# Kernel optimization log

Hardware: AMD Instinct MI355X
Metric: run time of the kernel (lower is better)

The kernel has to match this reference:

```python
import jax, jax.numpy as jnp
import numpy as np

TEMPERATURE = 0.1
NORM_EPS = 1e-12  # torch F.normalize clamps the norm at 1e-12


def _l2_normalize(x):
    n = jnp.sqrt(jnp.sum(x * x, axis=-1, keepdims=True))
    return x / jnp.maximum(n, NORM_EPS)


def setup_inputs() -> dict:
    key = jax.random.key(0)
    k1, k2 = jax.random.split(key)
    feat = jax.random.normal(k1, (32, 384, 28, 28), dtype=jnp.float32)
    codebook = jax.random.normal(k2, (2048, 384), dtype=jnp.float32)
    return {"feat": feat, "codebook": codebook}


def reference(feat, codebook):
    # feat: (b, c, h, w); codebook: (K, c)
    b, c, h, w = feat.shape
    K = codebook.shape[0]

    f = jnp.transpose(feat, (0, 2, 3, 1))          # (b, h, w, c), unnormalized
    flat = f.reshape(-1, c)                        # (N, c)
    flat_n = _l2_normalize(flat)                   # normalize=True
    code = _l2_normalize(codebook)                 # (K, c)

    distance = (jnp.sum(flat_n * flat_n, axis=1, keepdims=True)
                + jnp.sum(code * code, axis=1)
                - 2.0 * (flat_n @ code.T))

    # hard assignment (is_weight_sum=False): gather nearest code
    idx = jnp.argmin(distance, axis=1)             # (N,)
    q = code[idx]                                  # (N, c) == one_hot(idx) @ code
    q = q.reshape(b, h, w, c)

    # straight-through: gradient flows to f, not the quantized values
    q_feat = f + jax.lax.stop_gradient(q - f)      # (b, h, w, c)
    q_feat = jnp.transpose(q_feat, (0, 3, 1, 2))   # (b, c, h, w)

    prob = jax.nn.softmax(-distance / TEMPERATURE, axis=1)  # (N, K)
    assignment = jnp.transpose(prob.reshape(b, h, w, K), (0, 3, 1, 2))  # (b, K, h, w)

    return (f, q_feat, assignment, distance)
```

## Files before the change

kernel.cpp:

```cpp
#include <hip/hip_runtime.h>

#define B_  32
#define C_  384
#define HW_ 784
#define N_  25088
#define K_  2048
#define PPX 112

#define OFF_F    0
#define OFF_Q    9633792
#define OFF_ASG  19267584
#define OFF_DIST 70647808

#define MARGIN 0.02f

typedef unsigned short u16;
typedef unsigned int u32;
typedef __attribute__((ext_vector_type(8))) short short8;
typedef __attribute__((ext_vector_type(4))) float floatx4;

static __device__ __forceinline__ u16 f2bf(float x) {
    u32 u = __builtin_bit_cast(u32, x);
    u32 r = (u + 0x7FFFu + ((u >> 16) & 1u)) >> 16;
    return (u16)r;
}

static __device__ __forceinline__ void gload_lds16(const void* g, void* l) {
    __builtin_amdgcn_global_load_lds(
        (const __attribute__((address_space(1))) unsigned int*)g,
        (__attribute__((address_space(3))) unsigned int*)l,
        16, 0, 0);
}

static __device__ __forceinline__ size_t qslot(int b, int s, int hw) {
    return ((size_t)b * C_ + s) * HW_ + hw;
}

__global__ __launch_bounds__(256) void k_code(const float* __restrict__ cb,
                                              float* __restrict__ code_n,
                                              u16* __restrict__ b_hi) {
    int row  = blockIdx.x * 4 + (threadIdx.x >> 6);
    int lane = threadIdx.x & 63;
    const float* src = cb + (size_t)row * C_;
    float v[6];
    float ss = 0.f;
#pragma unroll
    for (int i = 0; i < 6; ++i) { v[i] = src[lane + 64 * i]; ss += v[i] * v[i]; }
#pragma unroll
    for (int off = 32; off; off >>= 1) ss += __shfl_xor(ss, off, 64);
    float inv = 1.f / fmaxf(sqrtf(ss), 1e-12f);
#pragma unroll
    for (int i = 0; i < 6; ++i) {
        float vn = v[i] * inv;
        code_n[(size_t)row * C_ + lane + 64 * i] = vn;
        b_hi  [(size_t)row * C_ + lane + 64 * i] = f2bf(vn);
    }
}

__global__ __launch_bounds__(256) void k_prep(const float* __restrict__ feat,
                                              float* __restrict__ f_out,
                                              float* __restrict__ inv_n,
                                              u16* __restrict__ a_hi) {
    __shared__ float tile[C_][17];
    __shared__ float red[16][17];
    __shared__ float s_inv[16];
    int b   = blockIdx.y;
    int hw0 = blockIdx.x * 16;
    int tid = threadIdx.x;
    int px  = tid & 15, cq = tid >> 4;

#pragma unroll
    for (int it = 0; it < 24; ++it) {
        int c = cq + 16 * it;
        tile[c][px] = feat[((size_t)(b * C_ + c)) * HW_ + hw0 + px];
    }
    __syncthreads();
    float ss = 0.f;
#pragma unroll
    for (int q = 0; q < 24; ++q) {
        float v = tile[cq + 16 * q][px];
        ss = fmaf(v, v, ss);
    }
    red[cq][px] = ss;
    __syncthreads();
    if (tid < 16) {
        float tot = 0.f;
#pragma unroll
        for (int p = 0; p < 16; ++p) tot += red[p][tid];
        float inv = 1.f / fmaxf(sqrtf(tot), 1e-12f);
        s_inv[tid] = inv;
        inv_n[(size_t)b * HW_ + hw0 + tid] = inv;
    }
    __syncthreads();

    {
        int p2 = tid >> 4, cc = tid & 15;
        float* fb = f_out + ((size_t)(b * HW_ + hw0 + p2)) * C_;
#pragma unroll
        for (int it = 0; it < 6; ++it) {
            int c0 = cc * 4 + 64 * it;
            float4 v;
            v.x = tile[c0 + 0][p2];
            v.y = tile[c0 + 1][p2];
            v.z = tile[c0 + 2][p2];
            v.w = tile[c0 + 3][p2];
            *(float4*)(fb + c0) = v;
        }
    }
    {
        int p2 = tid >> 4, cc = tid & 15;
        float inv = s_inv[p2];
        u16* aptr = a_hi + ((size_t)(b * HW_ + hw0 + p2)) * C_;
#pragma unroll
        for (int it = 0; it < 12; ++it) {
            int c0 = 2 * cc + 32 * it;
            u16 h0 = f2bf(tile[c0][p2] * inv);
            u16 h1 = f2bf(tile[c0 + 1][p2] * inv);
            *(u32*)(aptr + c0) = (u32)h0 | ((u32)h1 << 16);
        }
    }
}

__global__ __launch_bounds__(256) void k_gemm(const u16* __restrict__ A,
                                              const u16* __restrict__ Bm,
                                              float* __restrict__ D) {
    __shared__ u16 As[2][128 * 32];
    __shared__ u16 Bs[2][128 * 32];
    int tid = threadIdx.x;
    int n0 = blockIdx.x * 128, m0 = blockIdx.y * 128;
    int w = tid >> 6, l = tid & 63;
    int wm = (w >> 1) * 64, wn = (w & 1) * 64;
    int q4 = l >> 4, r15 = l & 15;

    floatx4 acc[4][4];
#pragma unroll
    for (int i = 0; i < 4; ++i)
#pragma unroll
        for (int j = 0; j < 4; ++j) acc[i][j] = (floatx4)0.f;

    int srow = tid >> 2;
    int sp   = tid & 3;
    int fs   = (srow ^ (srow >> 2)) & 3;
    int kk0  = 8 * (sp ^ fs);

#define STAGE(buf, kt)                                                          \
    {                                                                           \
        _Pragma("unroll")                                                       \
        for (int q = 0; q < 2; ++q) {                                           \
            int row = q * 64 + srow;                                            \
            int off = (q * 256 + tid) * 16;                                     \
            gload_lds16(A  + (size_t)(m0 + row) * C_ + (kt) + kk0,              \
                        (char*)As[buf] + off);                                  \
            gload_lds16(Bm + (size_t)(n0 + row) * C_ + (kt) + kk0,              \
                        (char*)Bs[buf] + off);                                  \
        }                                                                       \
    }

    STAGE(0, 0);
    __syncthreads();

    const int slot = (q4 ^ ((r15 ^ (r15 >> 2)) & 3)) << 4;
#pragma unroll 1
    for (int t = 0; t < 12; ++t) {
        int cur = t & 1;
        if (t < 11) STAGE(cur ^ 1, (t + 1) * 32);
        const char* Ab = (const char*)As[cur];
        const char* Bb = (const char*)Bs[cur];
        short8 a[4], b[4];
#pragma unroll
        for (int i = 0; i < 4; ++i) {
            a[i] = *(const short8*)(Ab + (wm + i * 16 + r15) * 64 + slot);
            b[i] = *(const short8*)(Bb + (wn + i * 16 + r15) * 64 + slot);
        }
#pragma unroll
        for (int i = 0; i < 4; ++i)
#pragma unroll
            for (int j = 0; j < 4; ++j)
                acc[i][j] = __builtin_amdgcn_mfma_f32_16x16x32_bf16(a[i], b[j], acc[i][j], 0, 0, 0);
        __syncthreads();
    }

#pragma unroll
    for (int i = 0; i < 4; ++i) {
        int gm = m0 + wm + i * 16 + q4 * 4;
#pragma unroll
        for (int j = 0; j < 4; ++j) {
            int gn = n0 + wn + j * 16 + r15;
            float* p = D + (size_t)gm * K_ + gn;
#pragma unroll
            for (int r = 0; r < 4; ++r)
                p[(size_t)r * K_] = 2.f - 2.f * acc[i][j][r];
        }
    }
#undef STAGE
}

__global__ __launch_bounds__(256) void k_stats(const float* __restrict__ D,
                                               float2* __restrict__ srow) {
    int row = blockIdx.x * 4 + (threadIdx.x >> 6);
    int l   = threadIdx.x & 63;
    const float* dr = D + (size_t)row * K_;
    float es = 0.f, dm = 3.4e38f;
#pragma unroll
    for (int i = 0; i < 8; ++i) {
        float4 v = *(const float4*)(dr + l * 4 + 256 * i);
        es += __expf(-10.f * v.x) + __expf(-10.f * v.y)
            + __expf(-10.f * v.z) + __expf(-10.f * v.w);
        dm = fminf(dm, fminf(fminf(v.x, v.y), fminf(v.z, v.w)));
    }
#pragma unroll
    for (int off = 32; off; off >>= 1) {
        es += __shfl_xor(es, off, 64);
        dm = fminf(dm, __shfl_xor(dm, off, 64));
    }
    if (l == 0) {
        float2 st;
        st.x = 1.f / es;
        st.y = dm + MARGIN;
        srow[row] = st;
    }
}

__global__ __launch_bounds__(256) void k_post(const float* __restrict__ D,
                                              const float2* __restrict__ srow,
                                              u32* __restrict__ Qi,
                                              float* __restrict__ asg) {
    __shared__ float tbuf[64][113];
    __shared__ float s_inv[PPX], s_thr[PPX];
    __shared__ int   s_cnt[PPX];
    __shared__ int   s_cand[PPX][16];
    int tile = blockIdx.x;
    int kc   = blockIdx.y;
    int b    = tile / 7;
    int hw0  = (tile - b * 7) * PPX;
    int n0   = b * HW_ + hw0;
    int tid  = threadIdx.x;

    if (tid < PPX) {
        float2 st = srow[n0 + tid];
        s_inv[tid] = st.x;
        s_thr[tid] = st.y;
        s_cnt[tid] = 0;
    }
    __syncthreads();

    int r16 = tid >> 4, c4 = (tid & 15) * 4;
    int px = tid & 127, kg = tid >> 7;
#pragma unroll 1
    for (int ch = 0; ch < 8; ++ch) {
        int k0 = kc * 512 + ch * 64;
#pragma unroll
        for (int rr = 0; rr < 7; ++rr) {
            int row = r16 + 16 * rr;
            float4 dv = *(const float4*)(D + (size_t)(n0 + row) * K_ + k0 + c4);
            float inv = s_inv[row], thr = s_thr[row];
            float dd[4] = {dv.x, dv.y, dv.z, dv.w};
#pragma unroll
            for (int cc = 0; cc < 4; ++cc) {
                float d = dd[cc];
                tbuf[c4 + cc][row] = __expf(-10.f * d) * inv;
                if (d <= thr) {
                    int idx = atomicAdd(&s_cnt[row], 1);
                    if (idx < 16) s_cand[row][idx] = k0 + c4 + cc;
                }
            }
        }
        __syncthreads();
        if (px < PPX) {
            size_t base = ((size_t)(b * K_ + k0 + kg * 32)) * HW_ + hw0 + px;
#pragma unroll
            for (int ki = 0; ki < 32; ++ki)
                asg[base + (size_t)ki * HW_] = tbuf[kg * 32 + ki][px];
        }
        __syncthreads();
    }

    if (tid < PPX) {
        int cnt = s_cnt[tid];
        cnt = cnt > 16 ? 16 : cnt;
        Qi[qslot(b, kc * 17, hw0 + tid)] = (u32)cnt;
        for (int ci = 0; ci < cnt; ++ci)
            Qi[qslot(b, kc * 17 + 1 + ci, hw0 + tid)] = (u32)s_cand[tid][ci];
    }
}

__global__ __launch_bounds__(256) void k_q(const u32* __restrict__ Qi,
                                           const float* __restrict__ codeN,
                                           const float* __restrict__ invN,
                                           const float* __restrict__ f_in,
                                           float* __restrict__ qOut) {
    __shared__ int s_amin[PPX], s_cnt[PPX];
    __shared__ int s_cand[PPX][64];
    int tile = blockIdx.x;
    int b    = tile / 7;
    int hw0  = (tile - b * 7) * PPX;
    int npix = b * HW_ + hw0;
    int tid  = threadIdx.x;

    if (tid < PPX) {
        int total = 0;
#pragma unroll
        for (int kc = 0; kc < 4; ++kc) {
            int cnt = (int)Qi[qslot(b, kc * 17, hw0 + tid)];
            for (int ci = 0; ci < cnt; ++ci)
                s_cand[tid][total++] = (int)Qi[qslot(b, kc * 17 + 1 + ci, hw0 + tid)];
        }
        s_cnt[tid]  = total;
        s_amin[tid] = s_cand[tid][0];
    }
    __syncthreads();

    int w = tid >> 6, l = tid & 63;
#pragma unroll 1
    for (int r = w; r < PPX; r += 4) {
        int cnt = s_cnt[r];
        if (cnt < 2) continue;
        float ivn = invN[npix + r];
        float fv[6];
        const float* frow = f_in + (size_t)(npix + r) * C_;
#pragma unroll
        for (int ii = 0; ii < 6; ++ii)
            fv[ii] = frow[l + 64 * ii] * ivn;
        float dbest = 3.4e38f;
        int   kbest = -1;
        for (int ci = 0; ci < cnt; ++ci) {
            int k = s_cand[r][ci];
            float dt = 0.f;
            const float* cr = codeN + (size_t)k * C_;
#pragma unroll
            for (int ii = 0; ii < 6; ++ii) dt = fmaf(fv[ii], cr[l + 64 * ii], dt);
#pragma unroll
            for (int off = 1; off < 64; off <<= 1) dt += __shfl_xor(dt, off, 64);
            float dex = 2.f - 2.f * dt;
            if (kbest < 0 || dex < dbest || (dex == dbest && k < kbest)) { dbest = dex; kbest = k; }
        }
        if (l == 0) s_amin[r] = kbest;
    }
    __syncthreads();

    int px = tid & 127, kg = tid >> 7;
    if (px < PPX) {
        const float* cr = codeN + (size_t)s_amin[px] * C_ + kg * 192;
        size_t qb = ((size_t)b * C_ + kg * 192) * HW_ + hw0 + px;
#pragma unroll 1
        for (int c4 = 0; c4 < 48; ++c4) {
            float4 v = *(const float4*)(cr + 4 * c4);
            qOut[qb + (size_t)(4 * c4 + 0) * HW_] = v.x;
            qOut[qb + (size_t)(4 * c4 + 1) * HW_] = v.y;
            qOut[qb + (size_t)(4 * c4 + 2) * HW_] = v.z;
            qOut[qb + (size_t)(4 * c4 + 3) * HW_] = v.w;
        }
    }
}

extern "C" void kernel_launch(void* const* d_in, const int* in_sizes, int n_in,
                              void* d_out, int out_size, void* d_ws, size_t ws_size,
                              hipStream_t stream) {
    const float* feat = (const float*)d_in[0];
    const float* cb   = (const float*)d_in[1];
    float* out    = (float*)d_out;
    float* f_out  = out + OFF_F;
    float* q_out  = out + OFF_Q;
    float* asg    = out + OFF_ASG;
    float* dist   = out + OFF_DIST;

    float*  code_n = (float*)d_ws;
    float*  inv_n  = (float*)((char*)d_ws + 3145728);
    float2* srow   = (float2*)((char*)d_ws + 3246080);

    u16* a_hi = (u16*)asg;
    u16* b_hi = a_hi + (size_t)N_ * C_;
    u32* Qi   = (u32*)q_out;

    k_code<<<K_ / 4, 256, 0, stream>>>(cb, code_n, b_hi);
    k_prep<<<dim3(HW_ / 16, B_), 256, 0, stream>>>(feat, f_out, inv_n, a_hi);
    k_gemm<<<dim3(K_ / 128, N_ / 128), 256, 0, stream>>>(a_hi, b_hi, dist);
    k_stats<<<N_ / 4, 256, 0, stream>>>(dist, srow);
    k_post<<<dim3(224, 4), 256, 0, stream>>>(dist, srow, Qi, asg);
    k_q<<<224, 256, 0, stream>>>(Qi, code_n, inv_n, f_out, q_out);
}
```

Baseline: 303.3 us.

## Fuse codebook prep into feature prep, swizzle GEMM tiles, use nontemporal stores

Merges the codebook normalization kernel into the feature prep kernel as extra blocks, which removes one launch. Remaps the GEMM block index with an 8-way swizzle so that concurrently running tiles share A/B rows in L2. Switches the large streaming outputs (f, assignment, q) and the distance reads in the post kernel to nontemporal loads and stores, to avoid polluting the cache. The swizzle changes the tile visit order, and nontemporal reads of the distance matrix, which was just written, could lose cache hits.

```diff
diff --git a/kernel.cpp b/kernel.cpp
--- a/kernel.cpp
+++ b/kernel.cpp
@@ -18,6 +18,7 @@
 typedef unsigned int u32;
 typedef __attribute__((ext_vector_type(8))) short short8;
 typedef __attribute__((ext_vector_type(4))) float floatx4;
+typedef __attribute__((ext_vector_type(4))) float f32x4;
 
 static __device__ __forceinline__ u16 f2bf(float x) {
     u32 u = __builtin_bit_cast(u32, x);
@@ -36,37 +37,38 @@
     return ((size_t)b * C_ + s) * HW_ + hw;
 }
 
-__global__ __launch_bounds__(256) void k_code(const float* __restrict__ cb,
+__global__ __launch_bounds__(256) void k_prep(const float* __restrict__ feat,
+                                              const float* __restrict__ cb,
+                                              float* __restrict__ f_out,
+                                              float* __restrict__ inv_n,
+                                              u16* __restrict__ a_hi,
                                               float* __restrict__ code_n,
                                               u16* __restrict__ b_hi) {
-    int row  = blockIdx.x * 4 + (threadIdx.x >> 6);
-    int lane = threadIdx.x & 63;
-    const float* src = cb + (size_t)row * C_;
-    float v[6];
-    float ss = 0.f;
-#pragma unroll
-    for (int i = 0; i < 6; ++i) { v[i] = src[lane + 64 * i]; ss += v[i] * v[i]; }
-#pragma unroll
-    for (int off = 32; off; off >>= 1) ss += __shfl_xor(ss, off, 64);
-    float inv = 1.f / fmaxf(sqrtf(ss), 1e-12f);
-#pragma unroll
-    for (int i = 0; i < 6; ++i) {
-        float vn = v[i] * inv;
-        code_n[(size_t)row * C_ + lane + 64 * i] = vn;
-        b_hi  [(size_t)row * C_ + lane + 64 * i] = f2bf(vn);
-    }
-}
-
-__global__ __launch_bounds__(256) void k_prep(const float* __restrict__ feat,
-                                              float* __restrict__ f_out,
-                                              float* __restrict__ inv_n,
-                                              u16* __restrict__ a_hi) {
+    int tid = threadIdx.x;
+    if (blockIdx.x >= 1568) {
+        int row  = (blockIdx.x - 1568) * 4 + (tid >> 6);
+        int lane = tid & 63;
+        const float* src = cb + (size_t)row * C_;
+        float v[6];
+        float ss = 0.f;
+#pragma unroll
+        for (int i = 0; i < 6; ++i) { v[i] = src[lane + 64 * i]; ss += v[i] * v[i]; }
+#pragma unroll
+        for (int off = 32; off; off >>= 1) ss += __shfl_xor(ss, off, 64);
+        float inv = 1.f / fmaxf(sqrtf(ss), 1e-12f);
+#pragma unroll
+        for (int i = 0; i < 6; ++i) {
+            float vn = v[i] * inv;
+            code_n[(size_t)row * C_ + lane + 64 * i] = vn;
+            b_hi  [(size_t)row * C_ + lane + 64 * i] = f2bf(vn);
+        }
+        return;
+    }
     __shared__ float tile[C_][17];
     __shared__ float red[16][17];
     __shared__ float s_inv[16];
-    int b   = blockIdx.y;
-    int hw0 = blockIdx.x * 16;
-    int tid = threadIdx.x;
+    int b   = blockIdx.x / 49;
+    int hw0 = (blockIdx.x - b * 49) * 16;
     int px  = tid & 15, cq = tid >> 4;
 
 #pragma unroll
@@ -99,12 +101,12 @@
 #pragma unroll
         for (int it = 0; it < 6; ++it) {
             int c0 = cc * 4 + 64 * it;
-            float4 v;
-            v.x = tile[c0 + 0][p2];
-            v.y = tile[c0 + 1][p2];
-            v.z = tile[c0 + 2][p2];
-            v.w = tile[c0 + 3][p2];
-            *(float4*)(fb + c0) = v;
+            f32x4 v;
+            v[0] = tile[c0 + 0][p2];
+            v[1] = tile[c0 + 1][p2];
+            v[2] = tile[c0 + 2][p2];
+            v[3] = tile[c0 + 3][p2];
+            __builtin_nontemporal_store(v, (f32x4*)(fb + c0));
         }
     }
     {
@@ -127,7 +129,10 @@
     __shared__ u16 As[2][128 * 32];
     __shared__ u16 Bs[2][128 * 32];
     int tid = threadIdx.x;
-    int n0 = blockIdx.x * 128, m0 = blockIdx.y * 128;
+    int lin = blockIdx.x;
+    int swz = (lin & 7) * 392 + (lin >> 3);
+    int n0 = (swz & 15) * 128;
+    int m0 = (swz >> 4) * 128;
     int w = tid >> 6, l = tid & 63;
     int wm = (w >> 1) * 64, wn = (w & 1) * 64;
     int q4 = l >> 4, r15 = l & 15;
@@ -252,12 +257,12 @@
 #pragma unroll
         for (int rr = 0; rr < 7; ++rr) {
             int row = r16 + 16 * rr;
-            float4 dv = *(const float4*)(D + (size_t)(n0 + row) * K_ + k0 + c4);
+            f32x4 dv = __builtin_nontemporal_load(
+                (const f32x4*)(D + (size_t)(n0 + row) * K_ + k0 + c4));
             float inv = s_inv[row], thr = s_thr[row];
-            float dd[4] = {dv.x, dv.y, dv.z, dv.w};
 #pragma unroll
             for (int cc = 0; cc < 4; ++cc) {
-                float d = dd[cc];
+                float d = dv[cc];
                 tbuf[c4 + cc][row] = __expf(-10.f * d) * inv;
                 if (d <= thr) {
                     int idx = atomicAdd(&s_cnt[row], 1);
@@ -270,7 +275,8 @@
             size_t base = ((size_t)(b * K_ + k0 + kg * 32)) * HW_ + hw0 + px;
 #pragma unroll
             for (int ki = 0; ki < 32; ++ki)
-                asg[base + (size_t)ki * HW_] = tbuf[kg * 32 + ki][px];
+                __builtin_nontemporal_store(tbuf[kg * 32 + ki][px],
+                                            asg + base + (size_t)ki * HW_);
         }
         __syncthreads();
     }
@@ -345,10 +351,10 @@
 #pragma unroll 1
         for (int c4 = 0; c4 < 48; ++c4) {
             float4 v = *(const float4*)(cr + 4 * c4);
-            qOut[qb + (size_t)(4 * c4 + 0) * HW_] = v.x;
-            qOut[qb + (size_t)(4 * c4 + 1) * HW_] = v.y;
-            qOut[qb + (size_t)(4 * c4 + 2) * HW_] = v.z;
-            qOut[qb + (size_t)(4 * c4 + 3) * HW_] = v.w;
+            __builtin_nontemporal_store(v.x, qOut + qb + (size_t)(4 * c4 + 0) * HW_);
+            __builtin_nontemporal_store(v.y, qOut + qb + (size_t)(4 * c4 + 1) * HW_);
+            __builtin_nontemporal_store(v.z, qOut + qb + (size_t)(4 * c4 + 2) * HW_);
+            __builtin_nontemporal_store(v.w, qOut + qb + (size_t)(4 * c4 + 3) * HW_);
         }
     }
 }
@@ -372,9 +378,8 @@
     u16* b_hi = a_hi + (size_t)N_ * C_;
     u32* Qi   = (u32*)q_out;
 
-    k_code<<<K_ / 4, 256, 0, stream>>>(cb, code_n, b_hi);
-    k_prep<<<dim3(HW_ / 16, B_), 256, 0, stream>>>(feat, f_out, inv_n, a_hi);
-    k_gemm<<<dim3(K_ / 128, N_ / 128), 256, 0, stream>>>(a_hi, b_hi, dist);
+    k_prep<<<2080, 256, 0, stream>>>(feat, cb, f_out, inv_n, a_hi, code_n, b_hi);
+    k_gemm<<<3136, 256, 0, stream>>>(a_hi, b_hi, dist);
     k_stats<<<N_ / 4, 256, 0, stream>>>(dist, srow);
     k_post<<<dim3(224, 4), 256, 0, stream>>>(dist, srow, Qi, asg);
     k_q<<<224, 256, 0, stream>>>(Qi, code_n, inv_n, f_out, q_out);
```

After: 258.1 us. 1.18x faster.
